# Optimization experiments

Hardware: AMD Instinct MI355X
Metric: run time of the kernel (lower is better)

Reference implementation:

```python
import jax, jax.numpy as jnp
import numpy as np

B, T, D = 64, 512, 1536   # batch, time, enc_size (2*768)
H = 30                    # z_rnn_size
L_SUP, R_SUP = -0.1, 1.1  # HardKuma stretched support
EPS = 1e-5


def setup_inputs() -> dict:
    key = jax.random.key(0)
    ks = jax.random.split(key, 12)
    s = 0.02
    return {
        "x": jax.random.normal(ks[0], (B, T, D), dtype=jnp.float32),
        "u": jax.random.uniform(ks[1], (B, T, 1), dtype=jnp.float32),
        # LSTMCell(enc_size + 1 -> H), torch gate order [i, f, g, o]
        "Wih": jax.random.normal(ks[2], (4 * H, D + 1), dtype=jnp.float32) * s,
        "Whh": jax.random.normal(ks[3], (4 * H, H), dtype=jnp.float32) * s,
        "bih": jax.random.normal(ks[4], (4 * H,), dtype=jnp.float32) * s,
        "bhh": jax.random.normal(ks[5], (4 * H,), dtype=jnp.float32) * s,
        # KumaGate: Linear(D + H -> 1) + Softplus for a and b
        "Wa": jax.random.normal(ks[6], (1, D + H), dtype=jnp.float32) * s,
        "ba": jax.random.normal(ks[7], (1,), dtype=jnp.float32) * s,
        "Wb": jax.random.normal(ks[8], (1, D + H), dtype=jnp.float32) * s,
        "bb": jax.random.normal(ks[9], (1,), dtype=jnp.float32) * s,
    }


def reference(x, u, Wih, Whh, bih, bhh, Wa, ba, Wb, bb):
    # x: [B, T, D], u: [B, T, 1] uniform reparam noise
    hseq = jnp.swapaxes(x, 0, 1)               # [T, B, D]
    useq = jnp.swapaxes(u, 0, 1)               # [T, B, 1]
    batch = x.shape[0]

    def step(carry, inp):
        hx, cx = carry                          # [B, H] each
        h_t, u_t = inp                          # [B, D], [B, 1]
        feat = jnp.concatenate([h_t, hx], axis=-1)          # [B, D+H]
        a = jnp.clip(jax.nn.softplus(feat @ Wa.T + ba), 1e-6, 100.0)
        b = jnp.clip(jax.nn.softplus(feat @ Wb.T + bb), 1e-6, 100.0)
        # HardKuma reparameterized sample (training branch)
        uu = jnp.clip(u_t, EPS, 1.0 - EPS)
        s = (1.0 - (1.0 - uu) ** (1.0 / b)) ** (1.0 / a)     # Kuma icdf
        t = s * (R_SUP - L_SUP) + L_SUP                      # stretch
        z_t = jnp.clip(t, 0.0, 1.0)                          # hard rectify, [B, 1]
        # LSTMCell update (torch gate order i, f, g, o)
        rnn_in = jnp.concatenate([h_t, z_t], axis=-1)        # [B, D+1]
        gates = rnn_in @ Wih.T + bih + hx @ Whh.T + bhh      # [B, 4H]
        i, f, g, o = jnp.split(gates, 4, axis=-1)
        c_new = jax.nn.sigmoid(f) * cx + jax.nn.sigmoid(i) * jnp.tanh(g)
        h_new = jax.nn.sigmoid(o) * jnp.tanh(c_new)
        return (h_new, c_new), z_t

    init = (jnp.zeros((batch, H), x.dtype), jnp.zeros((batch, H), x.dtype))
    _, zs = jax.lax.scan(step, init, (hseq, useq))           # zs: [T, B, 1]
    return jnp.swapaxes(zs[..., 0], 0, 1)                    # [B, T]
```

## Files before the change

### kernel.cpp

```cpp
#include <hip/hip_runtime.h>
#include <math.h>

#define Bb 64
#define Tt 512
#define Dd 1536
#define Hh 30
#define NC 128
#define Mm (Bb*Tt)
#define KSTEPS 48

typedef unsigned short u16;
typedef __attribute__((ext_vector_type(8))) short short8v;
typedef __attribute__((ext_vector_type(4))) float f32x4;

__device__ __forceinline__ float rcpf_(float x) { return __builtin_amdgcn_rcpf(x); }
__device__ __forceinline__ float sigmoidf_(float x) {
    return rcpf_(1.f + __expf(-x));
}
__device__ __forceinline__ float tanhf_fast(float x) {
    float e = __expf(2.f * x);
    return fmaf(-2.f, rcpf_(e + 1.f), 1.f);
}
__device__ __forceinline__ float softplus_(float x) {
    return fmaxf(x, 0.f) + __logf(1.f + __expf(-fabsf(x)));
}
__device__ __forceinline__ float rl_f(float v, int lane) {
    return __uint_as_float(__builtin_amdgcn_readlane(__float_as_uint(v), lane));
}

__device__ __forceinline__ f32x4 mm_bf16(short8v a, short8v b, f32x4 c) {
    return __builtin_amdgcn_mfma_f32_16x16x32_bf16(a, b, c, 0, 0, 0);
}

union U4S8 { unsigned int u[4]; short8v s; };

__device__ __forceinline__ void cvt_split(const float4 a, const float4 b,
                                          short8v& hi, short8v& lo) {
    float x[8] = {a.x, a.y, a.z, a.w, b.x, b.y, b.z, b.w};
    U4S8 H, L;
#pragma unroll
    for (int i = 0; i < 4; i++) {
        unsigned int u0 = __float_as_uint(x[2 * i]);
        unsigned int u1 = __float_as_uint(x[2 * i + 1]);
        unsigned int h0 = u0 & 0xffff0000u;
        unsigned int h1 = u1 & 0xffff0000u;
        H.u[i] = (u0 >> 16) | h1;
        float l0 = x[2 * i]     - __uint_as_float(h0);
        float l1 = x[2 * i + 1] - __uint_as_float(h1);
        L.u[i] = (__float_as_uint(l0) >> 16) | (__float_as_uint(l1) & 0xffff0000u);
    }
    hi = H.s;
    lo = L.s;
}

__global__ __launch_bounds__(256) void pack_w(const float* __restrict__ Wih,
                                              const float* __restrict__ Wa,
                                              const float* __restrict__ Wb,
                                              u16* __restrict__ Wbh,
                                              u16* __restrict__ Wbl) {
    const int k = blockIdx.x * 256 + threadIdx.x;
    const int c = blockIdx.y;
    float v = 0.f;
    if (c < 120)       v = Wih[c * (Dd + 1) + k];
    else if (c == 120) v = Wa[k];
    else if (c == 121) v = Wb[k];
    unsigned int u = __float_as_uint(v);
    unsigned int h = u & 0xffff0000u;
    float lo = v - __uint_as_float(h);
    Wbh[(size_t)c * Dd + k] = (u16)(u >> 16);
    Wbl[(size_t)c * Dd + k] = (u16)(__float_as_uint(lo) >> 16);
}

__global__ __launch_bounds__(256) void pack_s(const float* __restrict__ Wih,
                                              const float* __restrict__ Whh,
                                              const float* __restrict__ Wa,
                                              const float* __restrict__ Wb,
                                              float* __restrict__ WAp,
                                              float* __restrict__ WBp) {
    int t = threadIdx.x;
    for (int idx = t; idx < 64 * 32; idx += 256) {
        int l = idx >> 5, k = idx & 31;
        float va = 0.f, vb = 0.f;
        if (k < 30) {
            if (l < 30)                 { va = Whh[l * Hh + k];        vb = Whh[(30 + l) * Hh + k]; }
            else if (l == 30)           { va = Wa[Dd + k]; }
            else if (l == 31)           { va = Wb[Dd + k]; }
            else if (l < 62)            { va = Whh[(l + 28) * Hh + k]; vb = Whh[(l + 58) * Hh + k]; }
        } else if (k == 30) {
            if (l < 30)                 { va = Wih[l * (Dd + 1) + Dd];        vb = Wih[(30 + l) * (Dd + 1) + Dd]; }
            else if (l >= 32 && l < 62) { va = Wih[(l + 28) * (Dd + 1) + Dd]; vb = Wih[(l + 58) * (Dd + 1) + Dd]; }
        }
        WAp[idx] = va;
        WBp[idx] = vb;
    }
}

__global__ __launch_bounds__(256, 2) void gemm_k(const float* __restrict__ X,
                                                 const u16* __restrict__ Wbh,
                                                 const u16* __restrict__ Wbl,
                                                 const float* __restrict__ bih,
                                                 const float* __restrict__ bhh,
                                                 const float* __restrict__ ba,
                                                 const float* __restrict__ bbp,
                                                 float* __restrict__ GX) {
    const int t    = threadIdx.x;
    const int lane = t & 63;
    const int wid  = t >> 6;
    const int wrow = wid >> 1;
    const int wcol = wid & 1;
    const int m0   = blockIdx.x * 64 + wrow * 32;
    const int n0   = wcol * 64;
    const int lr   = lane & 15;
    const int lk   = lane >> 4;

    const float* xa0 = X + (size_t)(m0 + lr) * Dd + lk * 8;
    const float* xa1 = xa0 + (size_t)16 * Dd;
    const u16*   pbh = Wbh + (size_t)(n0 + lr) * Dd + lk * 8;
    const u16*   pbl = Wbl + (size_t)(n0 + lr) * Dd + lk * 8;

    f32x4 acc[2][4];
#pragma unroll
    for (int nt = 0; nt < 4; nt++) {
        int c = n0 + nt * 16 + lr;
        float bv = (c < 120) ? (bih[c] + bhh[c])
                 : (c == 120) ? ba[0]
                 : (c == 121) ? bbp[0] : 0.f;
        f32x4 v = {bv, bv, bv, bv};
        acc[0][nt] = v;
        acc[1][nt] = v;
    }

#define LOADA(ra, ks) do {                                        \
        ra[0] = *(const float4*)(xa0 + (ks) * 32);                \
        ra[1] = *(const float4*)(xa0 + (ks) * 32 + 4);            \
        ra[2] = *(const float4*)(xa1 + (ks) * 32);                \
        ra[3] = *(const float4*)(xa1 + (ks) * 32 + 4);            \
    } while (0)

#define LOADB(bh, bl, ks) do {                                               \
        _Pragma("unroll")                                                    \
        for (int nt = 0; nt < 4; nt++) {                                     \
            bh[nt] = *(const short8v*)(pbh + (size_t)nt * 16 * Dd + (ks) * 32); \
            bl[nt] = *(const short8v*)(pbl + (size_t)nt * 16 * Dd + (ks) * 32); \
        }                                                                    \
    } while (0)

#define STEP(ra, bh, bl) do {                                     \
        short8v ah0, al0, ah1, al1;                               \
        cvt_split(ra[0], ra[1], ah0, al0);                        \
        cvt_split(ra[2], ra[3], ah1, al1);                        \
        _Pragma("unroll")                                         \
        for (int nt = 0; nt < 4; nt++)                            \
            acc[0][nt] = mm_bf16(ah0, bh[nt], acc[0][nt]);        \
        _Pragma("unroll")                                         \
        for (int nt = 0; nt < 4; nt++)                            \
            acc[1][nt] = mm_bf16(ah1, bh[nt], acc[1][nt]);        \
        _Pragma("unroll")                                         \
        for (int nt = 0; nt < 4; nt++)                            \
            acc[0][nt] = mm_bf16(al0, bh[nt], acc[0][nt]);        \
        _Pragma("unroll")                                         \
        for (int nt = 0; nt < 4; nt++)                            \
            acc[1][nt] = mm_bf16(al1, bh[nt], acc[1][nt]);        \
        _Pragma("unroll")                                         \
        for (int nt = 0; nt < 4; nt++)                            \
            acc[0][nt] = mm_bf16(ah0, bl[nt], acc[0][nt]);        \
        _Pragma("unroll")                                         \
        for (int nt = 0; nt < 4; nt++)                            \
            acc[1][nt] = mm_bf16(ah1, bl[nt], acc[1][nt]);        \
    } while (0)

    float4  ra0[4], ra1[4];
    short8v bh0[4], bl0[4], bh1[4], bl1[4];

    LOADA(ra0, 0);
    LOADB(bh0, bl0, 0);
    int ks = 0;
    for (; ks < KSTEPS - 2; ks += 2) {
        LOADA(ra1, ks + 1);
        LOADB(bh1, bl1, ks + 1);
        STEP(ra0, bh0, bl0);
        LOADA(ra0, ks + 2);
        LOADB(bh0, bl0, ks + 2);
        STEP(ra1, bh1, bl1);
    }
    LOADA(ra1, KSTEPS - 1);
    LOADB(bh1, bl1, KSTEPS - 1);
    STEP(ra0, bh0, bl0);
    STEP(ra1, bh1, bl1);

#undef LOADA
#undef LOADB
#undef STEP

#pragma unroll
    for (int mt = 0; mt < 2; mt++)
#pragma unroll
        for (int nt = 0; nt < 4; nt++) {
            float* dst = GX + (size_t)(m0 + mt * 16 + lk * 4) * NC + n0 + nt * 16 + lr;
#pragma unroll
            for (int r = 0; r < 4; r++)
                dst[(size_t)r * NC] = acc[mt][nt][r];
        }
}

#define PIN16(A, B) asm volatile("" \
    : "+v"(A[B+0]), "+v"(A[B+1]), "+v"(A[B+2]),  "+v"(A[B+3]),  "+v"(A[B+4]),  "+v"(A[B+5]),  "+v"(A[B+6]),  "+v"(A[B+7]), \
      "+v"(A[B+8]), "+v"(A[B+9]), "+v"(A[B+10]), "+v"(A[B+11]), "+v"(A[B+12]), "+v"(A[B+13]), "+v"(A[B+14]), "+v"(A[B+15]))

__global__
__attribute__((amdgpu_flat_work_group_size(64, 64)))
__attribute__((amdgpu_waves_per_eu(1)))
void scan_k(const float* __restrict__ u,
            const float* __restrict__ gx,
            const float* __restrict__ WAp,
            const float* __restrict__ WBp,
            float* __restrict__ out) {
    __shared__ float lus[Tt];
    __shared__ float zbuf[Tt];
    const int b = blockIdx.x;
    const int l = threadIdx.x;

    for (int k = l; k < Tt; k += 64) {
        float uu = u[b * Tt + k];
        uu = fminf(fmaxf(uu, 1e-5f), 1.f - 1e-5f);
        lus[k] = __logf(1.f - uu);
    }
    __syncthreads();

    float wA[32], wB[32];
#pragma unroll
    for (int j = 0; j < 8; j++) {
        float4 a4 = ((const float4*)(WAp + l * 32))[j];
        float4 b4 = ((const float4*)(WBp + l * 32))[j];
        wA[4 * j + 0] = a4.x; wA[4 * j + 1] = a4.y; wA[4 * j + 2] = a4.z; wA[4 * j + 3] = a4.w;
        wB[4 * j + 0] = b4.x; wB[4 * j + 1] = b4.y; wB[4 * j + 2] = b4.z; wB[4 * j + 3] = b4.w;
    }

    int cA, cB;
    if (l < 30)       { cA = l;       cB = 30 + l; }
    else if (l == 30) { cA = 120;     cB = 122; }
    else if (l == 31) { cA = 121;     cB = 123; }
    else if (l < 62)  { cA = l + 28;  cB = l + 58; }
    else              { cA = 126;     cB = 127; }
    const float* gxb = gx + (size_t)b * Tt * NC;

    float h[Hh];
#pragma unroll
    for (int k = 0; k < Hh; k++) h[k] = 0.f;
    float cst = 0.f;

    float gA0 = gxb[cA], gB0 = gxb[cB];
    float gA1 = gxb[NC + cA], gB1 = gxb[NC + cB];
    float lu0 = lus[0], lu1 = lus[1];

    const int srcb = ((l & 31) + 32) << 2;

    for (int t = 0; t < Tt; t++) {
        PIN16(wA, 0); PIN16(wA, 16);
        PIN16(wB, 0); PIN16(wB, 16);

        float a0 = gA0, a1 = 0.f, a2 = 0.f, a3 = 0.f;
        float b0 = gB0, b1 = 0.f, b2 = 0.f, b3 = 0.f;
#pragma unroll
        for (int k = 0; k < 28; k += 4) {
            a0 = fmaf(wA[k], h[k], a0);         a1 = fmaf(wA[k + 1], h[k + 1], a1);
            a2 = fmaf(wA[k + 2], h[k + 2], a2); a3 = fmaf(wA[k + 3], h[k + 3], a3);
            b0 = fmaf(wB[k], h[k], b0);         b1 = fmaf(wB[k + 1], h[k + 1], b1);
            b2 = fmaf(wB[k + 2], h[k + 2], b2); b3 = fmaf(wB[k + 3], h[k + 3], b3);
        }
        a0 = fmaf(wA[28], h[28], a0); a1 = fmaf(wA[29], h[29], a1);
        b0 = fmaf(wB[28], h[28], b0); b1 = fmaf(wB[29], h[29], b1);
        float accA = (a0 + a2) + (a1 + a3);
        float accB = (b0 + b2) + (b1 + b3);

        gA0 = gA1; gB0 = gB1;
        float lu = lu0; lu0 = lu1;
        if (t + 2 < Tt) {
            gA1 = gxb[(size_t)(t + 2) * NC + cA];
            gB1 = gxb[(size_t)(t + 2) * NC + cB];
            lu1 = lus[t + 2];
        }

        const float av = rl_f(accA, 30);
        const float bv = rl_f(accA, 31);
        float a  = fminf(fmaxf(softplus_(av), 1e-6f), 100.f);
        float bk = fminf(fmaxf(softplus_(bv), 1e-6f), 100.f);
        float p = __expf(lu * rcpf_(bk));
        float inner = 1.f - p;
        float s = (inner <= 0.f) ? 0.f : __expf(__logf(inner) * rcpf_(a));
        float z = fminf(fmaxf(fmaf(1.2f, s, -0.1f), 0.f), 1.f);

        accA = fmaf(z, wA[30], accA);
        accB = fmaf(z, wB[30], accB);

        const float tg = tanhf_fast(accA);
        const float sA = sigmoidf_(accA);
        const float sB = sigmoidf_(accB);
        const float gg_t = __uint_as_float(__builtin_amdgcn_ds_bpermute(srcb, __float_as_uint(tg)));
        const float oo_s = __uint_as_float(__builtin_amdgcn_ds_bpermute(srcb, __float_as_uint(sB)));

        const float cn = fmaf(sB, cst, sA * gg_t);
        const float hn = oo_s * tanhf_fast(cn);
        cst = cn;
#pragma unroll
        for (int k = 0; k < Hh; k++) h[k] = rl_f(hn, k);
        if (l == 0) zbuf[t] = z;
    }
    __syncthreads();
    for (int k = l; k < Tt; k += 64) out[b * Tt + k] = zbuf[k];
}

extern "C" void kernel_launch(void* const* d_in, const int* in_sizes, int n_in,
                              void* d_out, int out_size, void* d_ws, size_t ws_size,
                              hipStream_t stream) {
    const float* x   = (const float*)d_in[0];
    const float* u   = (const float*)d_in[1];
    const float* Wih = (const float*)d_in[2];
    const float* Whh = (const float*)d_in[3];
    const float* bih = (const float*)d_in[4];
    const float* bhh = (const float*)d_in[5];
    const float* Wa  = (const float*)d_in[6];
    const float* ba  = (const float*)d_in[7];
    const float* Wb  = (const float*)d_in[8];
    const float* bbp = (const float*)d_in[9];
    float* out = (float*)d_out;

    char* wsb = (char*)d_ws;
    u16*   Wbh = (u16*)(wsb);
    u16*   Wbl = (u16*)(wsb + 393216);
    float* WAp = (float*)(wsb + 786432);
    float* WBp = (float*)(wsb + 794624);
    float* GX  = (float*)(wsb + 802816);

    pack_w<<<dim3(Dd / 256, NC), 256, 0, stream>>>(Wih, Wa, Wb, Wbh, Wbl);
    pack_s<<<1, 256, 0, stream>>>(Wih, Whh, Wa, Wb, WAp, WBp);
    gemm_k<<<Mm / 64, 256, 0, stream>>>(x, Wbh, Wbl, bih, bhh, ba, bbp, GX);
    scan_k<<<Bb, 64, 0, stream>>>(u, GX, WAp, WBp, out);
}
```

Measured before the change: 782.6 us.

## Compute Kuma a/b redundantly per half-wave and replace bpermute with permlane32 swap

Each half of the wavefront now computes its own dot product for the Kuma a (lanes 0-31) or b (lanes 32-63) pre-activation, then exchanges the softplus results with v_permlane32_swap instead of reading lanes 30/31 via readlane. The two ds_bpermute cross-half exchanges for the g and o gates are also replaced by permlane32_swap, which does not go through the LDS crossbar. The intent is to shorten the serial per-timestep critical path, since z no longer waits for the full gate accumulation plus readlanes. The cost is an extra 30-FMA dot product, 32 more weight registers and one more gx load per step.

Result: faster. 754.1 us (-3.6%).

```diff
diff --git a/kernel.cpp b/kernel.cpp
--- a/kernel.cpp
+++ b/kernel.cpp
@@ -12,6 +12,7 @@
 typedef unsigned short u16;
 typedef __attribute__((ext_vector_type(8))) short short8v;
 typedef __attribute__((ext_vector_type(4))) float f32x4;
+typedef unsigned int uint2v __attribute__((ext_vector_type(2)));
 
 __device__ __forceinline__ float rcpf_(float x) { return __builtin_amdgcn_rcpf(x); }
 __device__ __forceinline__ float sigmoidf_(float x) {
@@ -26,6 +27,16 @@
 }
 __device__ __forceinline__ float rl_f(float v, int lane) {
     return __uint_as_float(__builtin_amdgcn_readlane(__float_as_uint(v), lane));
+}
+
+__device__ __forceinline__ void plswap(float& x, float& y) {
+#if __has_builtin(__builtin_amdgcn_permlane32_swap)
+    uint2v r = __builtin_amdgcn_permlane32_swap(__float_as_uint(x), __float_as_uint(y), false, false);
+    x = __uint_as_float(r.x);
+    y = __uint_as_float(r.y);
+#else
+    asm volatile("v_permlane32_swap_b32 %0, %1" : "+v"(x), "+v"(y));
+#endif
 }
 
 __device__ __forceinline__ f32x4 mm_bf16(short8v a, short8v b, f32x4 c) {
@@ -227,13 +238,16 @@
     }
     __syncthreads();
 
-    float wA[32], wB[32];
+    float wA[32], wB[32], wZ[32];
+    const float* wzp = WAp + (l < 32 ? 30 : 31) * 32;
 #pragma unroll
     for (int j = 0; j < 8; j++) {
         float4 a4 = ((const float4*)(WAp + l * 32))[j];
         float4 b4 = ((const float4*)(WBp + l * 32))[j];
+        float4 z4 = ((const float4*)wzp)[j];
         wA[4 * j + 0] = a4.x; wA[4 * j + 1] = a4.y; wA[4 * j + 2] = a4.z; wA[4 * j + 3] = a4.w;
         wB[4 * j + 0] = b4.x; wB[4 * j + 1] = b4.y; wB[4 * j + 2] = b4.z; wB[4 * j + 3] = b4.w;
+        wZ[4 * j + 0] = z4.x; wZ[4 * j + 1] = z4.y; wZ[4 * j + 2] = z4.z; wZ[4 * j + 3] = z4.w;
     }
 
     int cA, cB;
@@ -242,6 +256,7 @@
     else if (l == 31) { cA = 121;     cB = 123; }
     else if (l < 62)  { cA = l + 28;  cB = l + 58; }
     else              { cA = 126;     cB = 127; }
+    const int cZ = (l < 32) ? 120 : 121;
     const float* gxb = gx + (size_t)b * Tt * NC;
 
     float h[Hh];
@@ -249,15 +264,30 @@
     for (int k = 0; k < Hh; k++) h[k] = 0.f;
     float cst = 0.f;
 
-    float gA0 = gxb[cA], gB0 = gxb[cB];
-    float gA1 = gxb[NC + cA], gB1 = gxb[NC + cB];
+    float gA0 = gxb[cA], gB0 = gxb[cB], gZ0 = gxb[cZ];
+    float gA1 = gxb[NC + cA], gB1 = gxb[NC + cB], gZ1 = gxb[NC + cZ];
     float lu0 = lus[0], lu1 = lus[1];
-
-    const int srcb = ((l & 31) + 32) << 2;
 
     for (int t = 0; t < Tt; t++) {
         PIN16(wA, 0); PIN16(wA, 16);
         PIN16(wB, 0); PIN16(wB, 16);
+        PIN16(wZ, 0); PIN16(wZ, 16);
+
+        float z0 = gZ0, z1 = 0.f, z2 = 0.f, z3 = 0.f;
+#pragma unroll
+        for (int k = 0; k < 28; k += 4) {
+            z0 = fmaf(wZ[k], h[k], z0);         z1 = fmaf(wZ[k + 1], h[k + 1], z1);
+            z2 = fmaf(wZ[k + 2], h[k + 2], z2); z3 = fmaf(wZ[k + 3], h[k + 3], z3);
+        }
+        z0 = fmaf(wZ[28], h[28], z0); z1 = fmaf(wZ[29], h[29], z1);
+        float zacc = (z0 + z2) + (z1 + z3);
+        float sp = softplus_(zacc);
+        float spA = sp, spB = sp;
+        plswap(spA, spB);
+        float a  = fminf(fmaxf(spA, 1e-6f), 100.f);
+        float bk = fminf(fmaxf(spB, 1e-6f), 100.f);
+
+        float lu = lu0;
 
         float a0 = gA0, a1 = 0.f, a2 = 0.f, a3 = 0.f;
         float b0 = gB0, b1 = 0.f, b2 = 0.f, b3 = 0.f;
@@ -273,18 +303,15 @@
         float accA = (a0 + a2) + (a1 + a3);
         float accB = (b0 + b2) + (b1 + b3);
 
-        gA0 = gA1; gB0 = gB1;
-        float lu = lu0; lu0 = lu1;
+        gA0 = gA1; gB0 = gB1; gZ0 = gZ1;
+        lu0 = lu1;
         if (t + 2 < Tt) {
             gA1 = gxb[(size_t)(t + 2) * NC + cA];
             gB1 = gxb[(size_t)(t + 2) * NC + cB];
+            gZ1 = gxb[(size_t)(t + 2) * NC + cZ];
             lu1 = lus[t + 2];
         }
 
-        const float av = rl_f(accA, 30);
-        const float bv = rl_f(accA, 31);
-        float a  = fminf(fmaxf(softplus_(av), 1e-6f), 100.f);
-        float bk = fminf(fmaxf(softplus_(bv), 1e-6f), 100.f);
         float p = __expf(lu * rcpf_(bk));
         float inner = 1.f - p;
         float s = (inner <= 0.f) ? 0.f : __expf(__logf(inner) * rcpf_(a));
@@ -293,11 +320,13 @@
         accA = fmaf(z, wA[30], accA);
         accB = fmaf(z, wB[30], accB);
 
-        const float tg = tanhf_fast(accA);
+        float tg = tanhf_fast(accA);
         const float sA = sigmoidf_(accA);
-        const float sB = sigmoidf_(accB);
-        const float gg_t = __uint_as_float(__builtin_amdgcn_ds_bpermute(srcb, __float_as_uint(tg)));
-        const float oo_s = __uint_as_float(__builtin_amdgcn_ds_bpermute(srcb, __float_as_uint(sB)));
+        float sB = sigmoidf_(accB);
+        float tgx = tg, gg_t = tg;
+        plswap(tgx, gg_t);
+        float sBx = sB, oo_s = sB;
+        plswap(sBx, oo_s);
 
         const float cn = fmaf(sB, cst, sA * gg_t);
         const float hn = oo_s * tanhf_fast(cn);
```

## Split LSTM scan across four waves with LDS hidden-state exchange

Applied to the files above, without the earlier changes.

The recurrent scan kernel moves from one wave per batch row to four waves, each owning 8 hidden units with one gate column per lane. Hidden state is exchanged through a double-buffered shared-memory array with a block barrier every timestep, and gates are gathered via ds_swizzle instead of bpermute. This halves the per-lane FMA work in the serial recurrence, at the cost of a __syncthreads and LDS round-trip on the critical path each step. The weight packing kernel is rewritten to match the new per-lane layout.

Result: faster. 662.1 us (-15.4%).

```diff
diff --git a/kernel.cpp b/kernel.cpp
--- a/kernel.cpp
+++ b/kernel.cpp
@@ -71,28 +71,30 @@
     Wbl[(size_t)c * Dd + k] = (u16)(__float_as_uint(lo) >> 16);
 }
 
-__global__ __launch_bounds__(256) void pack_s(const float* __restrict__ Wih,
-                                              const float* __restrict__ Whh,
-                                              const float* __restrict__ Wa,
-                                              const float* __restrict__ Wb,
-                                              float* __restrict__ WAp,
-                                              float* __restrict__ WBp) {
-    int t = threadIdx.x;
-    for (int idx = t; idx < 64 * 32; idx += 256) {
-        int l = idx >> 5, k = idx & 31;
-        float va = 0.f, vb = 0.f;
+__global__ __launch_bounds__(256) void pack_s2(const float* __restrict__ Wih,
+                                               const float* __restrict__ Whh,
+                                               const float* __restrict__ Wa,
+                                               const float* __restrict__ Wb,
+                                               float* __restrict__ WS2) {
+    const int tid = threadIdx.x;
+    const int w = tid >> 6, lane = tid & 63;
+    float v[32];
+#pragma unroll
+    for (int j = 0; j < 32; j++) v[j] = 0.f;
+    if (lane < 32) {
+        int g = lane >> 3, k = 8 * w + (lane & 7);
         if (k < 30) {
-            if (l < 30)                 { va = Whh[l * Hh + k];        vb = Whh[(30 + l) * Hh + k]; }
-            else if (l == 30)           { va = Wa[Dd + k]; }
-            else if (l == 31)           { va = Wb[Dd + k]; }
-            else if (l < 62)            { va = Whh[(l + 28) * Hh + k]; vb = Whh[(l + 58) * Hh + k]; }
-        } else if (k == 30) {
-            if (l < 30)                 { va = Wih[l * (Dd + 1) + Dd];        vb = Wih[(30 + l) * (Dd + 1) + Dd]; }
-            else if (l >= 32 && l < 62) { va = Wih[(l + 28) * (Dd + 1) + Dd]; vb = Wih[(l + 58) * (Dd + 1) + Dd]; }
-        }
-        WAp[idx] = va;
-        WBp[idx] = vb;
-    }
+            int cc = g * 30 + k;
+            for (int j = 0; j < 30; j++) v[j] = Whh[cc * Hh + j];
+            v[30] = Wih[cc * (Dd + 1) + Dd];
+        }
+    } else if (lane == 32) {
+        for (int j = 0; j < 30; j++) v[j] = Wa[Dd + j];
+    } else if (lane == 33) {
+        for (int j = 0; j < 30; j++) v[j] = Wb[Dd + j];
+    }
+    float* dst = WS2 + (size_t)tid * 32;
+    for (int j = 0; j < 32; j++) dst[j] = v[j];
 }
 
 __global__ __launch_bounds__(256, 2) void gemm_k(const float* __restrict__ X,
@@ -208,106 +210,113 @@
       "+v"(A[B+8]), "+v"(A[B+9]), "+v"(A[B+10]), "+v"(A[B+11]), "+v"(A[B+12]), "+v"(A[B+13]), "+v"(A[B+14]), "+v"(A[B+15]))
 
 __global__
-__attribute__((amdgpu_flat_work_group_size(64, 64)))
+__attribute__((amdgpu_flat_work_group_size(256, 256)))
 __attribute__((amdgpu_waves_per_eu(1)))
 void scan_k(const float* __restrict__ u,
             const float* __restrict__ gx,
-            const float* __restrict__ WAp,
-            const float* __restrict__ WBp,
+            const float* __restrict__ WS2,
             float* __restrict__ out) {
     __shared__ float lus[Tt];
     __shared__ float zbuf[Tt];
-    const int b = blockIdx.x;
-    const int l = threadIdx.x;
-
-    for (int k = l; k < Tt; k += 64) {
+    __shared__ float hb[2][32];
+    const int b   = blockIdx.x;
+    const int tid = threadIdx.x;
+    const int w   = tid >> 6;
+    const int lane = tid & 63;
+
+    for (int k = tid; k < Tt; k += 256) {
         float uu = u[b * Tt + k];
         uu = fminf(fmaxf(uu, 1e-5f), 1.f - 1e-5f);
         lus[k] = __logf(1.f - uu);
     }
+    if (tid < 64) ((float*)hb)[tid] = 0.f;
     __syncthreads();
 
-    float wA[32], wB[32];
-#pragma unroll
-    for (int j = 0; j < 8; j++) {
-        float4 a4 = ((const float4*)(WAp + l * 32))[j];
-        float4 b4 = ((const float4*)(WBp + l * 32))[j];
-        wA[4 * j + 0] = a4.x; wA[4 * j + 1] = a4.y; wA[4 * j + 2] = a4.z; wA[4 * j + 3] = a4.w;
-        wB[4 * j + 0] = b4.x; wB[4 * j + 1] = b4.y; wB[4 * j + 2] = b4.z; wB[4 * j + 3] = b4.w;
-    }
-
-    int cA, cB;
-    if (l < 30)       { cA = l;       cB = 30 + l; }
-    else if (l == 30) { cA = 120;     cB = 122; }
-    else if (l == 31) { cA = 121;     cB = 123; }
-    else if (l < 62)  { cA = l + 28;  cB = l + 58; }
-    else              { cA = 126;     cB = 127; }
-    const float* gxb = gx + (size_t)b * Tt * NC;
-
-    float h[Hh];
-#pragma unroll
-    for (int k = 0; k < Hh; k++) h[k] = 0.f;
+    float wv[32];
+    {
+        const float* wp = WS2 + (size_t)((w << 6) + lane) * 32;
+#pragma unroll
+        for (int j = 0; j < 8; j++) {
+            float4 v4 = ((const float4*)wp)[j];
+            wv[4 * j + 0] = v4.x; wv[4 * j + 1] = v4.y;
+            wv[4 * j + 2] = v4.z; wv[4 * j + 3] = v4.w;
+        }
+    }
+
+    int c;
+    if (lane < 32) { int g = lane >> 3, k = 8 * w + (lane & 7); c = (k < 30) ? g * 30 + k : 124; }
+    else if (lane == 32) c = 120;
+    else if (lane == 33) c = 121;
+    else c = 124;
+    const float* gxb = gx + (size_t)b * Tt * NC + c;
+
+    const bool isg = (lane < 32) && ((lane >> 3) == 2);
+
+    float h[32];
+#pragma unroll
+    for (int k = 0; k < 32; k++) h[k] = 0.f;
     float cst = 0.f;
 
-    float gA0 = gxb[cA], gB0 = gxb[cB];
-    float gA1 = gxb[NC + cA], gB1 = gxb[NC + cB];
+    float g0 = gxb[0];
+    float g1 = gxb[NC];
     float lu0 = lus[0], lu1 = lus[1];
 
-    const int srcb = ((l & 31) + 32) << 2;
-
     for (int t = 0; t < Tt; t++) {
-        PIN16(wA, 0); PIN16(wA, 16);
-        PIN16(wB, 0); PIN16(wB, 16);
-
-        float a0 = gA0, a1 = 0.f, a2 = 0.f, a3 = 0.f;
-        float b0 = gB0, b1 = 0.f, b2 = 0.f, b3 = 0.f;
+        PIN16(wv, 0); PIN16(wv, 16);
+
+        float a0 = g0, a1 = 0.f, a2 = 0.f, a3 = 0.f;
 #pragma unroll
         for (int k = 0; k < 28; k += 4) {
-            a0 = fmaf(wA[k], h[k], a0);         a1 = fmaf(wA[k + 1], h[k + 1], a1);
-            a2 = fmaf(wA[k + 2], h[k + 2], a2); a3 = fmaf(wA[k + 3], h[k + 3], a3);
-            b0 = fmaf(wB[k], h[k], b0);         b1 = fmaf(wB[k + 1], h[k + 1], b1);
-            b2 = fmaf(wB[k + 2], h[k + 2], b2); b3 = fmaf(wB[k + 3], h[k + 3], b3);
-        }
-        a0 = fmaf(wA[28], h[28], a0); a1 = fmaf(wA[29], h[29], a1);
-        b0 = fmaf(wB[28], h[28], b0); b1 = fmaf(wB[29], h[29], b1);
-        float accA = (a0 + a2) + (a1 + a3);
-        float accB = (b0 + b2) + (b1 + b3);
-
-        gA0 = gA1; gB0 = gB1;
-        float lu = lu0; lu0 = lu1;
-        if (t + 2 < Tt) {
-            gA1 = gxb[(size_t)(t + 2) * NC + cA];
-            gB1 = gxb[(size_t)(t + 2) * NC + cB];
-            lu1 = lus[t + 2];
-        }
-
-        const float av = rl_f(accA, 30);
-        const float bv = rl_f(accA, 31);
+            a0 = fmaf(wv[k], h[k], a0);         a1 = fmaf(wv[k + 1], h[k + 1], a1);
+            a2 = fmaf(wv[k + 2], h[k + 2], a2); a3 = fmaf(wv[k + 3], h[k + 3], a3);
+        }
+        a0 = fmaf(wv[28], h[28], a0); a1 = fmaf(wv[29], h[29], a1);
+        float acc = (a0 + a2) + (a1 + a3);
+
+        const float av = rl_f(acc, 32);
+        const float bv = rl_f(acc, 33);
         float a  = fminf(fmaxf(softplus_(av), 1e-6f), 100.f);
         float bk = fminf(fmaxf(softplus_(bv), 1e-6f), 100.f);
+        float lu = lu0;
         float p = __expf(lu * rcpf_(bk));
         float inner = 1.f - p;
         float s = (inner <= 0.f) ? 0.f : __expf(__logf(inner) * rcpf_(a));
         float z = fminf(fmaxf(fmaf(1.2f, s, -0.1f), 0.f), 1.f);
 
-        accA = fmaf(z, wA[30], accA);
-        accB = fmaf(z, wB[30], accB);
-
-        const float tg = tanhf_fast(accA);
-        const float sA = sigmoidf_(accA);
-        const float sB = sigmoidf_(accB);
-        const float gg_t = __uint_as_float(__builtin_amdgcn_ds_bpermute(srcb, __float_as_uint(tg)));
-        const float oo_s = __uint_as_float(__builtin_amdgcn_ds_bpermute(srcb, __float_as_uint(sB)));
-
-        const float cn = fmaf(sB, cst, sA * gg_t);
-        const float hn = oo_s * tanhf_fast(cn);
+        g0 = g1; lu0 = lu1;
+        if (t + 2 < Tt) {
+            g1 = gxb[(size_t)(t + 2) * NC];
+            lu1 = lus[t + 2];
+        }
+
+        acc = fmaf(z, wv[30], acc);
+
+        float tt = tanhf_fast(acc);
+        float ss = sigmoidf_(acc);
+        float val = isg ? tt : ss;
+
+        float vf = __uint_as_float(__builtin_amdgcn_ds_swizzle(__float_as_uint(val), 0x201F));
+        float vg = __uint_as_float(__builtin_amdgcn_ds_swizzle(__float_as_uint(val), 0x401F));
+        float vo = __uint_as_float(__builtin_amdgcn_ds_swizzle(__float_as_uint(val), 0x601F));
+
+        float cn = fmaf(vf, cst, val * vg);
+        float hn = vo * tanhf_fast(cn);
         cst = cn;
-#pragma unroll
-        for (int k = 0; k < Hh; k++) h[k] = rl_f(hn, k);
-        if (l == 0) zbuf[t] = z;
+
+        float* hbw = &hb[(t + 1) & 1][0];
+        if (lane < 8) hbw[8 * w + lane] = hn;
+        if (tid == 0) zbuf[t] = z;
+        __syncthreads();
+
+#pragma unroll
+        for (int j = 0; j < 8; j++) {
+            float4 h4 = ((const float4*)hbw)[j];
+            h[4 * j + 0] = h4.x; h[4 * j + 1] = h4.y;
+            h[4 * j + 2] = h4.z; h[4 * j + 3] = h4.w;
+        }
     }
     __syncthreads();
-    for (int k = l; k < Tt; k += 64) out[b * Tt + k] = zbuf[k];
+    for (int k = tid; k < Tt; k += 256) out[b * Tt + k] = zbuf[k];
 }
 
 extern "C" void kernel_launch(void* const* d_in, const int* in_sizes, int n_in,
@@ -328,12 +337,11 @@
     char* wsb = (char*)d_ws;
     u16*   Wbh = (u16*)(wsb);
     u16*   Wbl = (u16*)(wsb + 393216);
-    float* WAp = (float*)(wsb + 786432);
-    float* WBp = (float*)(wsb + 794624);
-    float* GX  = (float*)(wsb + 802816);
+    float* WS2 = (float*)(wsb + 786432);
+    float* GX  = (float*)(wsb + 819200);
 
     pack_w<<<dim3(Dd / 256, NC), 256, 0, stream>>>(Wih, Wa, Wb, Wbh, Wbl);
-    pack_s<<<1, 256, 0, stream>>>(Wih, Whh, Wa, Wb, WAp, WBp);
+    pack_s2<<<1, 256, 0, stream>>>(Wih, Whh, Wa, Wb, WS2);
     gemm_k<<<Mm / 64, 256, 0, stream>>>(x, Wbh, Wbl, bih, bhh, ba, bbp, GX);
-    scan_k<<<Bb, 64, 0, stream>>>(u, GX, WAp, WBp, out);
-}
+    scan_k<<<Bb, 256, 0, stream>>>(u, GX, WS2, out);
+}
```

## Remap LSTM scan gates to quad layout with DPP exchange and critical-path ordering

Applied to the files above, without the earlier changes.

Rearranges the recurrent weights so each quad of lanes holds the i, f, g, o gates of one hidden unit, with two hidden units per lane group. The gate exchange then uses DPP quad permutes instead of ds_bpermute through LDS. The kuma a/b dot product (wv1) is computed first so the z chain can overlap with the second dot product. The cost is more transcendental work per lane and extra selects for tanh versus sigmoid, and WS3 row 124 of the gx buffer is read for idle lanes.

Measured after the change: 666.4 us. 1.17x faster.

```diff
diff --git a/kernel.cpp b/kernel.cpp
--- a/kernel.cpp
+++ b/kernel.cpp
@@ -27,6 +27,9 @@
 __device__ __forceinline__ float rl_f(float v, int lane) {
     return __uint_as_float(__builtin_amdgcn_readlane(__float_as_uint(v), lane));
 }
+
+#define QPERM(src, CTRL) \
+    __uint_as_float((unsigned)__builtin_amdgcn_mov_dpp((int)__float_as_uint(src), CTRL, 0xF, 0xF, false))
 
 __device__ __forceinline__ f32x4 mm_bf16(short8v a, short8v b, f32x4 c) {
     return __builtin_amdgcn_mfma_f32_16x16x32_bf16(a, b, c, 0, 0, 0);
@@ -71,28 +74,32 @@
     Wbl[(size_t)c * Dd + k] = (u16)(__float_as_uint(lo) >> 16);
 }
 
-__global__ __launch_bounds__(256) void pack_s(const float* __restrict__ Wih,
+__global__ __launch_bounds__(64) void pack_s3(const float* __restrict__ Wih,
                                               const float* __restrict__ Whh,
                                               const float* __restrict__ Wa,
                                               const float* __restrict__ Wb,
-                                              float* __restrict__ WAp,
-                                              float* __restrict__ WBp) {
-    int t = threadIdx.x;
-    for (int idx = t; idx < 64 * 32; idx += 256) {
-        int l = idx >> 5, k = idx & 31;
-        float va = 0.f, vb = 0.f;
-        if (k < 30) {
-            if (l < 30)                 { va = Whh[l * Hh + k];        vb = Whh[(30 + l) * Hh + k]; }
-            else if (l == 30)           { va = Wa[Dd + k]; }
-            else if (l == 31)           { va = Wb[Dd + k]; }
-            else if (l < 62)            { va = Whh[(l + 28) * Hh + k]; vb = Whh[(l + 58) * Hh + k]; }
-        } else if (k == 30) {
-            if (l < 30)                 { va = Wih[l * (Dd + 1) + Dd];        vb = Wih[(30 + l) * (Dd + 1) + Dd]; }
-            else if (l >= 32 && l < 62) { va = Wih[(l + 28) * (Dd + 1) + Dd]; vb = Wih[(l + 58) * (Dd + 1) + Dd]; }
-        }
-        WAp[idx] = va;
-        WBp[idx] = vb;
-    }
+                                              float* __restrict__ WS3) {
+    const int l = threadIdx.x;
+    const int q = l >> 2, g = l & 3;
+    float v0[32], v1[32];
+#pragma unroll
+    for (int j = 0; j < 32; j++) { v0[j] = 0.f; v1[j] = 0.f; }
+    {
+        int c0 = g * 30 + q;
+        for (int j = 0; j < 30; j++) v0[j] = Whh[c0 * Hh + j];
+        v0[30] = Wih[c0 * (Dd + 1) + Dd];
+    }
+    if (q < 14) {
+        int c1 = g * 30 + 16 + q;
+        for (int j = 0; j < 30; j++) v1[j] = Whh[c1 * Hh + j];
+        v1[30] = Wih[c1 * (Dd + 1) + Dd];
+    } else if (l == 56) {
+        for (int j = 0; j < 30; j++) v1[j] = Wa[Dd + j];
+    } else if (l == 60) {
+        for (int j = 0; j < 30; j++) v1[j] = Wb[Dd + j];
+    }
+    float* dst = WS3 + (size_t)l * 64;
+    for (int j = 0; j < 32; j++) { dst[j] = v0[j]; dst[32 + j] = v1[j]; }
 }
 
 __global__ __launch_bounds__(256, 2) void gemm_k(const float* __restrict__ X,
@@ -212,13 +219,13 @@
 __attribute__((amdgpu_waves_per_eu(1)))
 void scan_k(const float* __restrict__ u,
             const float* __restrict__ gx,
-            const float* __restrict__ WAp,
-            const float* __restrict__ WBp,
+            const float* __restrict__ WS3,
             float* __restrict__ out) {
     __shared__ float lus[Tt];
     __shared__ float zbuf[Tt];
     const int b = blockIdx.x;
     const int l = threadIdx.x;
+    const int q = l >> 2, g = l & 3;
 
     for (int k = l; k < Tt; k += 64) {
         float uu = u[b * Tt + k];
@@ -227,83 +234,94 @@
     }
     __syncthreads();
 
-    float wA[32], wB[32];
-#pragma unroll
-    for (int j = 0; j < 8; j++) {
-        float4 a4 = ((const float4*)(WAp + l * 32))[j];
-        float4 b4 = ((const float4*)(WBp + l * 32))[j];
-        wA[4 * j + 0] = a4.x; wA[4 * j + 1] = a4.y; wA[4 * j + 2] = a4.z; wA[4 * j + 3] = a4.w;
-        wB[4 * j + 0] = b4.x; wB[4 * j + 1] = b4.y; wB[4 * j + 2] = b4.z; wB[4 * j + 3] = b4.w;
-    }
-
-    int cA, cB;
-    if (l < 30)       { cA = l;       cB = 30 + l; }
-    else if (l == 30) { cA = 120;     cB = 122; }
-    else if (l == 31) { cA = 121;     cB = 123; }
-    else if (l < 62)  { cA = l + 28;  cB = l + 58; }
-    else              { cA = 126;     cB = 127; }
-    const float* gxb = gx + (size_t)b * Tt * NC;
-
-    float h[Hh];
-#pragma unroll
-    for (int k = 0; k < Hh; k++) h[k] = 0.f;
-    float cst = 0.f;
-
-    float gA0 = gxb[cA], gB0 = gxb[cB];
-    float gA1 = gxb[NC + cA], gB1 = gxb[NC + cB];
+    float wv0[32], wv1[32];
+    {
+        const float* wp = WS3 + (size_t)l * 64;
+#pragma unroll
+        for (int j = 0; j < 8; j++) {
+            float4 a4 = ((const float4*)wp)[j];
+            float4 b4 = ((const float4*)(wp + 32))[j];
+            wv0[4 * j + 0] = a4.x; wv0[4 * j + 1] = a4.y;
+            wv0[4 * j + 2] = a4.z; wv0[4 * j + 3] = a4.w;
+            wv1[4 * j + 0] = b4.x; wv1[4 * j + 1] = b4.y;
+            wv1[4 * j + 2] = b4.z; wv1[4 * j + 3] = b4.w;
+        }
+    }
+
+    const int c0 = g * 30 + q;
+    const int c1 = (q < 14) ? (g * 30 + 16 + q) : ((l == 56) ? 120 : (l == 60) ? 121 : 124);
+    const float* p0 = gx + (size_t)b * Tt * NC + c0;
+    const float* p1 = gx + (size_t)b * Tt * NC + c1;
+
+    float hs[Hh];
+#pragma unroll
+    for (int k = 0; k < Hh; k++) hs[k] = 0.f;
+    float cst0 = 0.f, cst1 = 0.f;
+
+    float A0 = p0[0], B0 = p1[0];
+    float A1 = p0[NC], B1 = p1[NC];
     float lu0 = lus[0], lu1 = lus[1];
 
-    const int srcb = ((l & 31) + 32) << 2;
-
     for (int t = 0; t < Tt; t++) {
-        PIN16(wA, 0); PIN16(wA, 16);
-        PIN16(wB, 0); PIN16(wB, 16);
-
-        float a0 = gA0, a1 = 0.f, a2 = 0.f, a3 = 0.f;
-        float b0 = gB0, b1 = 0.f, b2 = 0.f, b3 = 0.f;
+        PIN16(wv0, 0); PIN16(wv0, 16);
+        PIN16(wv1, 0); PIN16(wv1, 16);
+
+        float d10 = B0, d11 = 0.f, d12 = 0.f, d13 = 0.f;
 #pragma unroll
         for (int k = 0; k < 28; k += 4) {
-            a0 = fmaf(wA[k], h[k], a0);         a1 = fmaf(wA[k + 1], h[k + 1], a1);
-            a2 = fmaf(wA[k + 2], h[k + 2], a2); a3 = fmaf(wA[k + 3], h[k + 3], a3);
-            b0 = fmaf(wB[k], h[k], b0);         b1 = fmaf(wB[k + 1], h[k + 1], b1);
-            b2 = fmaf(wB[k + 2], h[k + 2], b2); b3 = fmaf(wB[k + 3], h[k + 3], b3);
-        }
-        a0 = fmaf(wA[28], h[28], a0); a1 = fmaf(wA[29], h[29], a1);
-        b0 = fmaf(wB[28], h[28], b0); b1 = fmaf(wB[29], h[29], b1);
-        float accA = (a0 + a2) + (a1 + a3);
-        float accB = (b0 + b2) + (b1 + b3);
-
-        gA0 = gA1; gB0 = gB1;
-        float lu = lu0; lu0 = lu1;
-        if (t + 2 < Tt) {
-            gA1 = gxb[(size_t)(t + 2) * NC + cA];
-            gB1 = gxb[(size_t)(t + 2) * NC + cB];
-            lu1 = lus[t + 2];
-        }
-
-        const float av = rl_f(accA, 30);
-        const float bv = rl_f(accA, 31);
+            d10 = fmaf(wv1[k], hs[k], d10);         d11 = fmaf(wv1[k + 1], hs[k + 1], d11);
+            d12 = fmaf(wv1[k + 2], hs[k + 2], d12); d13 = fmaf(wv1[k + 3], hs[k + 3], d13);
+        }
+        d10 = fmaf(wv1[28], hs[28], d10); d11 = fmaf(wv1[29], hs[29], d11);
+        float dot1 = (d10 + d12) + (d11 + d13);
+
+        const float av = rl_f(dot1, 56);
+        const float bv = rl_f(dot1, 60);
         float a  = fminf(fmaxf(softplus_(av), 1e-6f), 100.f);
         float bk = fminf(fmaxf(softplus_(bv), 1e-6f), 100.f);
+        float lu = lu0;
         float p = __expf(lu * rcpf_(bk));
         float inner = 1.f - p;
         float s = (inner <= 0.f) ? 0.f : __expf(__logf(inner) * rcpf_(a));
         float z = fminf(fmaxf(fmaf(1.2f, s, -0.1f), 0.f), 1.f);
 
-        accA = fmaf(z, wA[30], accA);
-        accB = fmaf(z, wB[30], accB);
-
-        const float tg = tanhf_fast(accA);
-        const float sA = sigmoidf_(accA);
-        const float sB = sigmoidf_(accB);
-        const float gg_t = __uint_as_float(__builtin_amdgcn_ds_bpermute(srcb, __float_as_uint(tg)));
-        const float oo_s = __uint_as_float(__builtin_amdgcn_ds_bpermute(srcb, __float_as_uint(sB)));
-
-        const float cn = fmaf(sB, cst, sA * gg_t);
-        const float hn = oo_s * tanhf_fast(cn);
-        cst = cn;
-#pragma unroll
-        for (int k = 0; k < Hh; k++) h[k] = rl_f(hn, k);
+        float d00 = A0, d01 = 0.f, d02 = 0.f, d03 = 0.f;
+#pragma unroll
+        for (int k = 0; k < 28; k += 4) {
+            d00 = fmaf(wv0[k], hs[k], d00);         d01 = fmaf(wv0[k + 1], hs[k + 1], d01);
+            d02 = fmaf(wv0[k + 2], hs[k + 2], d02); d03 = fmaf(wv0[k + 3], hs[k + 3], d03);
+        }
+        d00 = fmaf(wv0[28], hs[28], d00); d01 = fmaf(wv0[29], hs[29], d01);
+        float dot0 = (d00 + d02) + (d01 + d03);
+
+        A0 = A1; B0 = B1; lu0 = lu1;
+        if (t + 2 < Tt) {
+            A1 = p0[(size_t)(t + 2) * NC];
+            B1 = p1[(size_t)(t + 2) * NC];
+            lu1 = lus[t + 2];
+        }
+
+        float acc0 = fmaf(z, wv0[30], dot0);
+        float acc1 = fmaf(z, wv1[30], dot1);
+
+        float val0 = (g == 2) ? tanhf_fast(acc0) : sigmoidf_(acc0);
+        float val1 = (g == 2) ? tanhf_fast(acc1) : sigmoidf_(acc1);
+
+        float vf0 = QPERM(val0, 0x55), vg0 = QPERM(val0, 0xAA), vo0 = QPERM(val0, 0xFF);
+        float vf1 = QPERM(val1, 0x55), vg1 = QPERM(val1, 0xAA), vo1 = QPERM(val1, 0xFF);
+
+        float cn0 = fmaf(vf0, cst0, val0 * vg0);
+        float hn0 = vo0 * tanhf_fast(cn0);
+        cst0 = cn0;
+        float cn1 = fmaf(vf1, cst1, val1 * vg1);
+        float hn1 = vo1 * tanhf_fast(cn1);
+        cst1 = cn1;
+
+#pragma unroll
+        for (int k = 0; k < 16; k++) hs[k] = rl_f(hn0, 4 * k);
+#pragma unroll
+        for (int k = 16; k < Hh; k++) hs[k] = rl_f(hn1, 4 * (k - 16));
+
         if (l == 0) zbuf[t] = z;
     }
     __syncthreads();
@@ -328,12 +346,11 @@
     char* wsb = (char*)d_ws;
     u16*   Wbh = (u16*)(wsb);
     u16*   Wbl = (u16*)(wsb + 393216);
-    float* WAp = (float*)(wsb + 786432);
-    float* WBp = (float*)(wsb + 794624);
+    float* WS3 = (float*)(wsb + 786432);
     float* GX  = (float*)(wsb + 802816);
 
     pack_w<<<dim3(Dd / 256, NC), 256, 0, stream>>>(Wih, Wa, Wb, Wbh, Wbl);
-    pack_s<<<1, 256, 0, stream>>>(Wih, Whh, Wa, Wb, WAp, WBp);
+    pack_s3<<<1, 64, 0, stream>>>(Wih, Whh, Wa, Wb, WS3);
     gemm_k<<<Mm / 64, 256, 0, stream>>>(x, Wbh, Wbl, bih, bhh, ba, bbp, GX);
-    scan_k<<<Bb, 64, 0, stream>>>(u, GX, WAp, WBp, out);
-}
+    scan_k<<<Bb, 64, 0, stream>>>(u, GX, WS3, out);
+}
```
